# Kernel optimization log

Hardware: AMD Instinct MI355X
Metric: run time of the kernel (lower is better)

## Reference

```python
import jax, jax.numpy as jnp
import numpy as np

B, T, DM, H, DK, DV = 2, 2048, 1024, 16, 64, 64


def setup_inputs() -> dict:
    key = jax.random.key(0)
    k = jax.random.split(key, 7)
    std_k = np.float32(1.0 / np.sqrt(DK))
    std_v = np.float32(1.0 / np.sqrt(DV))
    return {
        "xq": jax.random.normal(k[0], (B, T, DM), jnp.float32),
        "xk": jax.random.normal(k[1], (B, T, DM), jnp.float32),
        "xv": jax.random.normal(k[2], (B, T, DM), jnp.float32),
        "mask": jnp.ones((B, T), jnp.float32),  # padding mask: 1 = keep
        "w_q": jax.random.normal(k[3], (H, DM, DK), jnp.float32) * std_k,
        "w_k": jax.random.normal(k[4], (H, DM, DK), jnp.float32) * std_k,
        "w_v": jax.random.normal(k[5], (H, DM, DV), jnp.float32) * std_v,
        "w_o": jax.random.normal(k[6], (H * DV, DM), jnp.float32) * np.float32(1.0 / np.sqrt(H * DV)),
        "b_o": jnp.zeros((DM,), jnp.float32),
    }


def reference(xq, xk, xv, mask, w_q, w_k, w_v, w_o, b_o):
    d_k = w_q.shape[-1]
    # per-head projections: [B,T,DM] x [H,DM,DK] -> [B,H,T,DK]
    q = jnp.einsum('bsd,hdk->bhsk', xq, w_q)
    kk = jnp.einsum('btd,hdk->bhtk', xk, w_k)
    v = jnp.einsum('btd,hdv->bhtv', xv, w_v)
    # NOTE: source divides by d_k (not sqrt(d_k)) -- kept faithful
    scores = jnp.einsum('bhsk,bhtk->bhst', q, kk) / jnp.float32(d_k)
    # _padding_mask: multiply by mask broadcast over key dim, then any exact
    # zero (masked OR coincidentally zero score) becomes -inf -- kept faithful
    masked = scores * mask[:, None, None, :]
    scores = jnp.where(masked == 0.0, -jnp.inf, masked)
    attn = jax.nn.softmax(scores, axis=-1)
    out = jnp.einsum('bhst,bhtv->bhsv', attn, v)  # [B,H,T,DV]
    b, h, t, dv = out.shape
    concat = out.transpose(0, 2, 1, 3).reshape(b, t, h * dv)
    return concat @ w_o + b_o
```

## Files before the change

### kernel.cpp

```cpp
#include <hip/hip_runtime.h>
#include <hip/hip_bf16.h>


typedef __attribute__((ext_vector_type(8))) short short8;
typedef __attribute__((ext_vector_type(4))) short short4v;
typedef __attribute__((ext_vector_type(4))) float f32x4;
typedef __attribute__((ext_vector_type(4))) int i32x4;

__device__ __forceinline__ short f2bf(float f) {
  union { float f; unsigned u; } v; v.f = f;
  unsigned r = v.u + 0x7FFFu + ((v.u >> 16) & 1u);
  return (short)(r >> 16);
}

#define GLD_LDS(g, l) __builtin_amdgcn_global_load_lds( \
    (const __attribute__((address_space(1))) void*)(g), \
    (__attribute__((address_space(3))) void*)(l), 16, 0, 0)

__global__ __launch_bounds__(256) void prep_all(
    const float* __restrict__ xq, const float* __restrict__ xk,
    const float* __restrict__ xv, const float* __restrict__ wq,
    const float* __restrict__ wk, const float* __restrict__ wv,
    const float* __restrict__ wo,
    short* __restrict__ Xb, short* __restrict__ Wall, short* __restrict__ Wot)
{
  const int bx = blockIdx.x, tid = threadIdx.x;
  __shared__ float Lt[64][65];
  if (bx < 6144) {
    int z = bx >> 11;
    const float* x = z == 0 ? xq : (z == 1 ? xk : xv);
    size_t i = ((size_t)(bx & 2047) * 256 + tid) * 8;
    f32x4 f0 = *(const f32x4*)(x + i);
    f32x4 f1 = *(const f32x4*)(x + i + 4);
    short8 s;
#pragma unroll
    for (int j = 0; j < 4; j++) { s[j] = f2bf(f0[j]); s[4 + j] = f2bf(f1[j]); }
    *(short8*)(Xb + (size_t)z * 4194304 + i) = s;
  } else if (bx < 6912) {
    int bz = bx - 6144;
    int z = bz >> 8, inner = bz & 255;
    const float* w = z == 0 ? wq : (z == 1 ? wk : wv);
    short* Wt = Wall + (size_t)z * 1048576;
    int h = inner >> 4, d0 = (inner & 15) * 64;
#pragma unroll
    for (int it = 0; it < 4; it++) {
      int e = tid + it * 256;
      int dl = e >> 4, k4 = (e & 15) * 4;
      f32x4 v = *(const f32x4*)(w + ((size_t)(h * 1024 + d0 + dl) * 64) + k4);
#pragma unroll
      for (int j = 0; j < 4; j++) Lt[dl][k4 + j] = v[j];
    }
    __syncthreads();
#pragma unroll
    for (int it = 0; it < 4; it++) {
      int e = tid + it * 256;
      int kl = e >> 4, dq = e & 15;
      short4v s;
#pragma unroll
      for (int j = 0; j < 4; j++) s[j] = f2bf(Lt[dq * 4 + j][kl]);
      *(short4v*)(Wt + (size_t)(h * 64 + kl) * 1024 + d0 + dq * 4) = s;
    }
  } else {
    int bz = bx - 6912;
    int k0 = (bz >> 4) * 64, n0 = (bz & 15) * 64;
#pragma unroll
    for (int it = 0; it < 4; it++) {
      int e = tid + it * 256;
      int kl = e >> 4, n4 = (e & 15) * 4;
      f32x4 v = *(const f32x4*)(wo + (size_t)(k0 + kl) * 1024 + n0 + n4);
#pragma unroll
      for (int j = 0; j < 4; j++) Lt[kl][n4 + j] = v[j];
    }
    __syncthreads();
#pragma unroll
    for (int it = 0; it < 4; it++) {
      int e = tid + it * 256;
      int nl = e >> 4, kq = e & 15;
      short4v s;
#pragma unroll
      for (int j = 0; j < 4; j++) s[j] = f2bf(Lt[kq * 4 + j][nl]);
      *(short4v*)(Wot + (size_t)(n0 + nl) * 1024 + k0 + kq * 4) = s;
    }
  }
}

__global__ __launch_bounds__(256) void proj_qkv3(
    const short* __restrict__ Xb, const short* __restrict__ Wall,
    short* __restrict__ Qb, short* __restrict__ Kt2, short* __restrict__ Vt2)
{
  const int z = blockIdx.z;
  const short* X  = Xb   + (size_t)z * 4194304;
  const short* Wt = Wall + (size_t)z * 1048576;

  const int t0 = blockIdx.x * 128;
  const int n0 = blockIdx.y * 128;
  const int tid = threadIdx.x, w = tid >> 6, lane = tid & 63;
  const int c = lane & 15, q4 = lane >> 4;
  const int wn = (w & 1) * 64, wt = (w >> 1) * 64;
  const int srow = lane >> 2, scol = (lane & 3) * 8;

  __shared__ __align__(16) short Al[2][2][4096];
  __shared__ __align__(16) short Bl[2][2][4096];

  f32x4 acc[4][4] = {};

#define PSTAGE(BUF, K0) do { \
    _Pragma("unroll") \
    for (int sub = 0; sub < 2; sub++) { \
      _Pragma("unroll") \
      for (int i = 0; i < 2; i++) { \
        int rg = (w * 2 + i) * 16; \
        GLD_LDS(Wt + (size_t)(n0 + rg + srow) * 1024 + (K0) + sub * 32 + scol, &Al[BUF][sub][rg * 32]); \
        GLD_LDS(X  + (size_t)(t0 + rg + srow) * 1024 + (K0) + sub * 32 + scol, &Bl[BUF][sub][rg * 32]); \
      } \
    } \
  } while (0)

#define PCOMP(BUF) do { \
    _Pragma("unroll") \
    for (int sub = 0; sub < 2; sub++) { \
      short8 a[4], bfr[4]; \
      if (z != 2) { \
        _Pragma("unroll") \
        for (int i = 0; i < 4; i++) \
          a[i] = *(const short8*)(&Al[BUF][sub][(wn + i * 16 + c) * 32 + q4 * 8]); \
        _Pragma("unroll") \
        for (int j = 0; j < 4; j++) \
          bfr[j] = *(const short8*)(&Bl[BUF][sub][(wt + j * 16 + c) * 32 + q4 * 8]); \
      } else { \
        _Pragma("unroll") \
        for (int i = 0; i < 4; i++) \
          a[i] = *(const short8*)(&Bl[BUF][sub][(wt + i * 16 + c) * 32 + q4 * 8]); \
        _Pragma("unroll") \
        for (int j = 0; j < 4; j++) \
          bfr[j] = *(const short8*)(&Al[BUF][sub][(wn + j * 16 + c) * 32 + q4 * 8]); \
      } \
      _Pragma("unroll") \
      for (int i = 0; i < 4; i++) \
        _Pragma("unroll") \
        for (int j = 0; j < 4; j++) \
          acc[i][j] = __builtin_amdgcn_mfma_f32_16x16x32_bf16(a[i], bfr[j], acc[i][j], 0, 0, 0); \
    } \
  } while (0)

  PSTAGE(0, 0);
  asm volatile("s_waitcnt vmcnt(0)" ::: "memory");
  __syncthreads();
  int cur = 0;
  for (int p = 0; p < 15; ++p) {
    PSTAGE(cur ^ 1, (p + 1) * 64);
    PCOMP(cur);
    asm volatile("s_waitcnt vmcnt(0)" ::: "memory");
    __syncthreads();
    cur ^= 1;
  }
  PCOMP(cur);
#undef PSTAGE
#undef PCOMP

  if (z != 2) {
#pragma unroll
    for (int i = 0; i < 4; i++)
#pragma unroll
      for (int j = 0; j < 4; j++) {
        int n = n0 + wn + i * 16 + q4 * 4;
        int trow = t0 + wt + j * 16 + c;
        int b = trow >> 11, t = trow & 2047;
        int h = n >> 6, cc = n & 63;
        int bh = b * 16 + h;
        f32x4 v = acc[i][j];
        short4v pk;
#pragma unroll
        for (int r = 0; r < 4; r++) pk[r] = f2bf(v[r]);
        if (z == 0) {
          *(short4v*)(Qb + (size_t)(bh * 2048 + t) * 64 + cc) = pk;
        } else {
          int t5 = t & 31, s_ = t5 >> 4, c_ = t5 & 15;
          size_t base = (size_t)bh * 131072 + (t >> 5) * 2048;
          size_t off = base + ((s_ * 2 + (cc >> 5)) * 16 + c_) * 32 +
                       ((cc >> 3) & 3) * 8 + (cc & 7);
          *(short4v*)(Kt2 + off) = pk;
        }
      }
  } else {
#pragma unroll
    for (int i = 0; i < 4; i++)
#pragma unroll
      for (int j = 0; j < 4; j++) {
        int tq = t0 + wt + i * 16 + q4 * 4;
        int n = n0 + wn + j * 16 + c;
        int b = tq >> 11, t = tq & 2047;
        int h = n >> 6, cc = n & 63;
        int bh = b * 16 + h;
        int t5 = t & 31;
        int kpb = ((t5 >> 2) & 3) * 8 + ((t5 >> 4) & 1) * 4;
        size_t base = (size_t)bh * 131072 + (t >> 5) * 2048;
        f32x4 v = acc[i][j];
        short4v pk;
#pragma unroll
        for (int r = 0; r < 4; r++) pk[r] = f2bf(v[r]);
        *(short4v*)(Vt2 + base + (size_t)cc * 32 + kpb) = pk;
      }
  }
}

__global__ __launch_bounds__(256, 2) void attn14(
    const short* __restrict__ Qb, const short* __restrict__ Kt2,
    const short* __restrict__ Vt2, const float* __restrict__ mask,
    short* __restrict__ AO)
{
  const int bh = blockIdx.x;
  const int tblk = blockIdx.y;
  const int b = bh >> 4, h = bh & 15;
  const short* Qh = Qb  + (size_t)bh * 131072;
  const short* Kh = Kt2 + (size_t)bh * 131072;
  const short* Vh = Vt2 + (size_t)bh * 131072;

  const int tid = threadIdx.x, w = tid >> 6, lane = tid & 63;
  const int c = lane & 15, q4 = lane >> 4;
  const int qrow0 = tblk * 128 + w * 32;

  __shared__ __align__(16) short KV2[2][8192];
  __shared__ __align__(16) float cmL[2048];
  __shared__ __align__(16) float cbL[2048];

  const int ch = c * 4 + q4;
  const int rdo = (ch ^ ((ch >> 3) & 3)) * 8;
  const int sch = (lane ^ ((lane >> 3) & 3)) * 8;

  {
    const float LOG2E_64c = 1.44269504088896f * 0.015625f;
    f32x4 m0 = *(const f32x4*)(mask + b * 2048 + tid * 8);
    f32x4 m1 = *(const f32x4*)(mask + b * 2048 + tid * 8 + 4);
    *(f32x4*)(&cmL[tid * 8])     = m0 * LOG2E_64c;
    *(f32x4*)(&cmL[tid * 8 + 4]) = m1 * LOG2E_64c;
    *(f32x4*)(&cbL[tid * 8])     = (m0 - 1.0f) * 240.0f;
    *(f32x4*)(&cbL[tid * 8 + 4]) = (m1 - 1.0f) * 240.0f;
  }

  short8 qa[2][2];
#pragma unroll
  for (int u = 0; u < 2; u++)
#pragma unroll
    for (int dc = 0; dc < 2; dc++)
      qa[u][dc] = *(const short8*)(Qh + (size_t)(qrow0 + u * 16 + c) * 64 + dc * 32 + q4 * 8);

  f32x4 acc[2][4] = {};
  float l[2] = {0.f, 0.f};

  const int g0 = w * 2;

#define STAGE(BI, P) do { \
    const short* s0 = (g0 < 4) ? (Kh + (size_t)(2 * (P)) * 2048 + g0 * 512) \
                               : (Vh + (size_t)(2 * (P)) * 2048 + (g0 - 4) * 512); \
    GLD_LDS(s0 + sch,         &KV2[BI][g0 * 512]); \
    GLD_LDS(s0 + 512 + sch,   &KV2[BI][g0 * 512 + 512]); \
    const short* s1 = (g0 < 4) ? (Kh + (size_t)(2 * (P) + 1) * 2048 + g0 * 512) \
                               : (Vh + (size_t)(2 * (P) + 1) * 2048 + (g0 - 4) * 512); \
    GLD_LDS(s1 + sch,         &KV2[BI][4096 + g0 * 512]); \
    GLD_LDS(s1 + 512 + sch,   &KV2[BI][4096 + g0 * 512 + 512]); \
  } while (0)

#define BODY1(KB, TT) do { \
    const short* Kb = (KB); \
    short8 kf[2][2], va[4]; \
    _Pragma("unroll") \
    for (int s = 0; s < 2; s++) \
      _Pragma("unroll") \
      for (int dc = 0; dc < 2; dc++) \
        kf[s][dc] = *(const short8*)(Kb + (s * 2 + dc) * 512 + rdo); \
    _Pragma("unroll") \
    for (int vs = 0; vs < 4; vs++) \
      va[vs] = *(const short8*)(Kb + 2048 + vs * 512 + rdo); \
    f32x4 st[2][2]; \
    _Pragma("unroll") \
    for (int u = 0; u < 2; u++) \
      _Pragma("unroll") \
      for (int s = 0; s < 2; s++) { \
        f32x4 z = {}; \
        z = __builtin_amdgcn_mfma_f32_16x16x32_bf16(kf[s][0], qa[u][0], z, 0, 0, 0); \
        st[u][s] = __builtin_amdgcn_mfma_f32_16x16x32_bf16(kf[s][1], qa[u][1], z, 0, 0, 0); \
      } \
    f32x4 cm[2], cb[2]; \
    _Pragma("unroll") \
    for (int s = 0; s < 2; s++) { \
      cm[s] = *(const f32x4*)(&cmL[(TT) * 32 + q4 * 4 + s * 16]); \
      cb[s] = *(const f32x4*)(&cbL[(TT) * 32 + q4 * 4 + s * 16]); \
    } \
    _Pragma("unroll") \
    for (int u = 0; u < 2; u++) { \
      unsigned pkd[2][2]; \
      _Pragma("unroll") \
      for (int s = 0; s < 2; s++) { \
        float e0 = __builtin_amdgcn_exp2f(st[u][s][0] * cm[s][0] + cb[s][0]); \
        float e1 = __builtin_amdgcn_exp2f(st[u][s][1] * cm[s][1] + cb[s][1]); \
        float e2 = __builtin_amdgcn_exp2f(st[u][s][2] * cm[s][2] + cb[s][2]); \
        float e3 = __builtin_amdgcn_exp2f(st[u][s][3] * cm[s][3] + cb[s][3]); \
        l[u] += (e0 + e1) + (e2 + e3); \
        unsigned p01, p23; \
        asm("v_cvt_pk_bf16_f32 %0, %1, %2" : "=v"(p01) : "v"(e0), "v"(e1)); \
        asm("v_cvt_pk_bf16_f32 %0, %1, %2" : "=v"(p23) : "v"(e2), "v"(e3)); \
        pkd[s][0] = p01; pkd[s][1] = p23; \
      } \
      union { i32x4 i; short8 s; } pb; \
      pb.i[0] = (int)pkd[0][0]; pb.i[1] = (int)pkd[0][1]; \
      pb.i[2] = (int)pkd[1][0]; pb.i[3] = (int)pkd[1][1]; \
      _Pragma("unroll") \
      for (int vs = 0; vs < 4; vs++) \
        acc[u][vs] = __builtin_amdgcn_mfma_f32_16x16x32_bf16(va[vs], pb.s, acc[u][vs], 0, 0, 0); \
    } \
  } while (0)

#define BODY(BI, P) do { \
    BODY1(&KV2[BI][0],    2 * (P)); \
    BODY1(&KV2[BI][4096], 2 * (P) + 1); \
  } while (0)

  __syncthreads();
  asm volatile("s_waitcnt vmcnt(0)" ::: "memory");
  STAGE(0, 0);
  asm volatile("s_waitcnt vmcnt(0)" ::: "memory");
  __syncthreads();
  int cur = 0;
  for (int p = 0; p < 31; ++p) {
    STAGE(cur ^ 1, p + 1);
    BODY(cur, p);
    asm volatile("s_waitcnt vmcnt(0)" ::: "memory");
    __syncthreads();
    cur ^= 1;
  }
  BODY(cur, 31);
#undef STAGE
#undef BODY1
#undef BODY

#pragma unroll
  for (int u = 0; u < 2; u++) {
    float lu = l[u];
    lu += __shfl_xor(lu, 16);
    lu += __shfl_xor(lu, 32);
    float inv = 1.0f / lu;
    size_t row = (size_t)b * 2048 + qrow0 + u * 16 + c;
#pragma unroll
    for (int vs = 0; vs < 4; vs++) {
      f32x4 v = acc[u][vs];
      short4v pk;
#pragma unroll
      for (int r = 0; r < 4; r++) pk[r] = f2bf(v[r] * inv);
      *(short4v*)(AO + row * 1024 + h * 64 + vs * 16 + q4 * 4) = pk;
    }
  }
}

__global__ __launch_bounds__(256) void out_proj3(
    const short* __restrict__ AO, const short* __restrict__ Wot,
    const float* __restrict__ bo, float* __restrict__ out)
{
  const int t0 = blockIdx.x * 128;
  const int n0 = blockIdx.y * 128;
  const int tid = threadIdx.x, w = tid >> 6, lane = tid & 63;
  const int c = lane & 15, q4 = lane >> 4;
  const int wn = (w & 1) * 64, wt = (w >> 1) * 64;
  const int srow = lane >> 2, scol = (lane & 3) * 8;

  __shared__ __align__(16) short Al[2][2][4096];
  __shared__ __align__(16) short Bl[2][2][4096];

  f32x4 acc[4][4] = {};

#define PSTAGE(BUF, K0) do { \
    _Pragma("unroll") \
    for (int sub = 0; sub < 2; sub++) { \
      _Pragma("unroll") \
      for (int i = 0; i < 2; i++) { \
        int rg = (w * 2 + i) * 16; \
        GLD_LDS(Wot + (size_t)(n0 + rg + srow) * 1024 + (K0) + sub * 32 + scol, &Al[BUF][sub][rg * 32]); \
        GLD_LDS(AO  + (size_t)(t0 + rg + srow) * 1024 + (K0) + sub * 32 + scol, &Bl[BUF][sub][rg * 32]); \
      } \
    } \
  } while (0)

#define PCOMP(BUF) do { \
    _Pragma("unroll") \
    for (int sub = 0; sub < 2; sub++) { \
      short8 a[4], bfr[4]; \
      _Pragma("unroll") \
      for (int i = 0; i < 4; i++) \
        a[i] = *(const short8*)(&Al[BUF][sub][(wn + i * 16 + c) * 32 + q4 * 8]); \
      _Pragma("unroll") \
      for (int j = 0; j < 4; j++) \
        bfr[j] = *(const short8*)(&Bl[BUF][sub][(wt + j * 16 + c) * 32 + q4 * 8]); \
      _Pragma("unroll") \
      for (int i = 0; i < 4; i++) \
        _Pragma("unroll") \
        for (int j = 0; j < 4; j++) \
          acc[i][j] = __builtin_amdgcn_mfma_f32_16x16x32_bf16(a[i], bfr[j], acc[i][j], 0, 0, 0); \
    } \
  } while (0)

  PSTAGE(0, 0);
  asm volatile("s_waitcnt vmcnt(0)" ::: "memory");
  __syncthreads();
  int cur = 0;
  for (int p = 0; p < 15; ++p) {
    PSTAGE(cur ^ 1, (p + 1) * 64);
    PCOMP(cur);
    asm volatile("s_waitcnt vmcnt(0)" ::: "memory");
    __syncthreads();
    cur ^= 1;
  }
  PCOMP(cur);
#undef PSTAGE
#undef PCOMP

#pragma unroll
  for (int i = 0; i < 4; i++)
#pragma unroll
    for (int j = 0; j < 4; j++) {
      int n = n0 + wn + i * 16 + q4 * 4;
      int trow = t0 + wt + j * 16 + c;
      f32x4 v = acc[i][j] + *(const f32x4*)(bo + n);
      *(f32x4*)(out + (size_t)trow * 1024 + n) = v;
    }
}

extern "C" void kernel_launch(void* const* d_in, const int* in_sizes, int n_in,
                              void* d_out, int out_size, void* d_ws, size_t ws_size,
                              hipStream_t stream)
{
  (void)in_sizes; (void)n_in; (void)out_size; (void)ws_size;
  const float* xq   = (const float*)d_in[0];
  const float* xk   = (const float*)d_in[1];
  const float* xv   = (const float*)d_in[2];
  const float* mask = (const float*)d_in[3];
  const float* wq   = (const float*)d_in[4];
  const float* wk   = (const float*)d_in[5];
  const float* wv   = (const float*)d_in[6];
  const float* wo   = (const float*)d_in[7];
  const float* bo   = (const float*)d_in[8];
  float* out = (float*)d_out;

  char* ws = (char*)d_ws;
  short* Wall = (short*)(ws + (size_t)0);
  short* Wot  = (short*)(ws + ((size_t)6 << 20));
  short* Xb   = (short*)(ws + ((size_t)8 << 20));
  short* AO   = (short*)(ws + ((size_t)8 << 20));
  short* Qb   = (short*)(ws + ((size_t)32 << 20));
  short* Kt2  = (short*)(ws + ((size_t)40 << 20));
  short* Vt2  = (short*)(ws + ((size_t)48 << 20));

  prep_all<<<7168, 256, 0, stream>>>(xq, xk, xv, wq, wk, wv, wo, Xb, Wall, Wot);
  proj_qkv3<<<dim3(32, 8, 3), 256, 0, stream>>>(Xb, Wall, Qb, Kt2, Vt2);
  attn14<<<dim3(32, 16), 256, 0, stream>>>(Qb, Kt2, Vt2, mask, AO);
  out_proj3<<<dim3(32, 8), 256, 0, stream>>>(AO, Wot, bo, out);
}
```

Before: 217.9 us.

## Fuse fp32-to-bf16 activation conversion into QKV projection staging

Removes the separate activation conversion pass from the prep kernel and instead loads fp32 activations directly in the projection GEMM. They go into registers, are converted with packed bf16 instructions, and are written to LDS after the MFMA compute, which keeps the double-buffered pipeline. This avoids writing and re-reading a 24MB bf16 copy of the inputs. In exchange each projection block reads fp32 activations (twice the bytes) once per N-tile, across 8 N-tiles. It also uses more registers and no longer uses async global-to-LDS loads for the X operand.

```diff
diff --git a/kernel.cpp b/kernel.cpp
--- a/kernel.cpp
+++ b/kernel.cpp
@@ -17,28 +17,15 @@
     (const __attribute__((address_space(1))) void*)(g), \
     (__attribute__((address_space(3))) void*)(l), 16, 0, 0)
 
-__global__ __launch_bounds__(256) void prep_all(
-    const float* __restrict__ xq, const float* __restrict__ xk,
-    const float* __restrict__ xv, const float* __restrict__ wq,
-    const float* __restrict__ wk, const float* __restrict__ wv,
-    const float* __restrict__ wo,
-    short* __restrict__ Xb, short* __restrict__ Wall, short* __restrict__ Wot)
+__global__ __launch_bounds__(256) void prep_w(
+    const float* __restrict__ wq, const float* __restrict__ wk,
+    const float* __restrict__ wv, const float* __restrict__ wo,
+    short* __restrict__ Wall, short* __restrict__ Wot)
 {
   const int bx = blockIdx.x, tid = threadIdx.x;
   __shared__ float Lt[64][65];
-  if (bx < 6144) {
-    int z = bx >> 11;
-    const float* x = z == 0 ? xq : (z == 1 ? xk : xv);
-    size_t i = ((size_t)(bx & 2047) * 256 + tid) * 8;
-    f32x4 f0 = *(const f32x4*)(x + i);
-    f32x4 f1 = *(const f32x4*)(x + i + 4);
-    short8 s;
-#pragma unroll
-    for (int j = 0; j < 4; j++) { s[j] = f2bf(f0[j]); s[4 + j] = f2bf(f1[j]); }
-    *(short8*)(Xb + (size_t)z * 4194304 + i) = s;
-  } else if (bx < 6912) {
-    int bz = bx - 6144;
-    int z = bz >> 8, inner = bz & 255;
+  if (bx < 768) {
+    int z = bx >> 8, inner = bx & 255;
     const float* w = z == 0 ? wq : (z == 1 ? wk : wv);
     short* Wt = Wall + (size_t)z * 1048576;
     int h = inner >> 4, d0 = (inner & 15) * 64;
@@ -61,7 +48,7 @@
       *(short4v*)(Wt + (size_t)(h * 64 + kl) * 1024 + d0 + dq * 4) = s;
     }
   } else {
-    int bz = bx - 6912;
+    int bz = bx - 768;
     int k0 = (bz >> 4) * 64, n0 = (bz & 15) * 64;
 #pragma unroll
     for (int it = 0; it < 4; it++) {
@@ -84,12 +71,13 @@
   }
 }
 
-__global__ __launch_bounds__(256) void proj_qkv3(
-    const short* __restrict__ Xb, const short* __restrict__ Wall,
+__global__ __launch_bounds__(256) void proj_qkv4(
+    const float* __restrict__ xq, const float* __restrict__ xk,
+    const float* __restrict__ xv, const short* __restrict__ Wall,
     short* __restrict__ Qb, short* __restrict__ Kt2, short* __restrict__ Vt2)
 {
   const int z = blockIdx.z;
-  const short* X  = Xb   + (size_t)z * 4194304;
+  const float* X  = z == 0 ? xq : (z == 1 ? xk : xv);
   const short* Wt = Wall + (size_t)z * 1048576;
 
   const int t0 = blockIdx.x * 128;
@@ -103,15 +91,44 @@
   __shared__ __align__(16) short Bl[2][2][4096];
 
   f32x4 acc[4][4] = {};
-
-#define PSTAGE(BUF, K0) do { \
+  f32x4 xr[2][2][2];
+
+#define PSTAGE_A(BUF, K0) do { \
     _Pragma("unroll") \
     for (int sub = 0; sub < 2; sub++) { \
       _Pragma("unroll") \
       for (int i = 0; i < 2; i++) { \
         int rg = (w * 2 + i) * 16; \
         GLD_LDS(Wt + (size_t)(n0 + rg + srow) * 1024 + (K0) + sub * 32 + scol, &Al[BUF][sub][rg * 32]); \
-        GLD_LDS(X  + (size_t)(t0 + rg + srow) * 1024 + (K0) + sub * 32 + scol, &Bl[BUF][sub][rg * 32]); \
+      } \
+    } \
+  } while (0)
+
+#define XLOAD(K0) do { \
+    _Pragma("unroll") \
+    for (int i = 0; i < 2; i++) { \
+      _Pragma("unroll") \
+      for (int sub = 0; sub < 2; sub++) { \
+        const float* xs = X + (size_t)(t0 + (w * 2 + i) * 16 + srow) * 1024 + (K0) + sub * 32 + scol; \
+        xr[i][sub][0] = *(const f32x4*)(xs); \
+        xr[i][sub][1] = *(const f32x4*)(xs + 4); \
+      } \
+    } \
+  } while (0)
+
+#define XWRITE(BUF) do { \
+    _Pragma("unroll") \
+    for (int i = 0; i < 2; i++) { \
+      _Pragma("unroll") \
+      for (int sub = 0; sub < 2; sub++) { \
+        unsigned p0, p1, p2, p3; \
+        asm("v_cvt_pk_bf16_f32 %0, %1, %2" : "=v"(p0) : "v"(xr[i][sub][0][0]), "v"(xr[i][sub][0][1])); \
+        asm("v_cvt_pk_bf16_f32 %0, %1, %2" : "=v"(p1) : "v"(xr[i][sub][0][2]), "v"(xr[i][sub][0][3])); \
+        asm("v_cvt_pk_bf16_f32 %0, %1, %2" : "=v"(p2) : "v"(xr[i][sub][1][0]), "v"(xr[i][sub][1][1])); \
+        asm("v_cvt_pk_bf16_f32 %0, %1, %2" : "=v"(p3) : "v"(xr[i][sub][1][2]), "v"(xr[i][sub][1][3])); \
+        union { i32x4 iv; short8 s; } pk; \
+        pk.iv[0] = (int)p0; pk.iv[1] = (int)p1; pk.iv[2] = (int)p2; pk.iv[3] = (int)p3; \
+        *(short8*)(&Bl[BUF][sub][((w * 2 + i) * 16 + srow) * 32 + scol]) = pk.s; \
       } \
     } \
   } while (0)
@@ -143,19 +160,25 @@
     } \
   } while (0)
 
-  PSTAGE(0, 0);
+  PSTAGE_A(0, 0);
+  XLOAD(0);
+  XWRITE(0);
   asm volatile("s_waitcnt vmcnt(0)" ::: "memory");
   __syncthreads();
   int cur = 0;
   for (int p = 0; p < 15; ++p) {
-    PSTAGE(cur ^ 1, (p + 1) * 64);
+    PSTAGE_A(cur ^ 1, (p + 1) * 64);
+    XLOAD((p + 1) * 64);
     PCOMP(cur);
+    XWRITE(cur ^ 1);
     asm volatile("s_waitcnt vmcnt(0)" ::: "memory");
     __syncthreads();
     cur ^= 1;
   }
   PCOMP(cur);
-#undef PSTAGE
+#undef PSTAGE_A
+#undef XLOAD
+#undef XWRITE
 #undef PCOMP
 
   if (z != 2) {
@@ -443,14 +466,13 @@
   char* ws = (char*)d_ws;
   short* Wall = (short*)(ws + (size_t)0);
   short* Wot  = (short*)(ws + ((size_t)6 << 20));
-  short* Xb   = (short*)(ws + ((size_t)8 << 20));
   short* AO   = (short*)(ws + ((size_t)8 << 20));
-  short* Qb   = (short*)(ws + ((size_t)32 << 20));
-  short* Kt2  = (short*)(ws + ((size_t)40 << 20));
-  short* Vt2  = (short*)(ws + ((size_t)48 << 20));
-
-  prep_all<<<7168, 256, 0, stream>>>(xq, xk, xv, wq, wk, wv, wo, Xb, Wall, Wot);
-  proj_qkv3<<<dim3(32, 8, 3), 256, 0, stream>>>(Xb, Wall, Qb, Kt2, Vt2);
+  short* Qb   = (short*)(ws + ((size_t)16 << 20));
+  short* Kt2  = (short*)(ws + ((size_t)24 << 20));
+  short* Vt2  = (short*)(ws + ((size_t)32 << 20));
+
+  prep_w<<<1024, 256, 0, stream>>>(wq, wk, wv, wo, Wall, Wot);
+  proj_qkv4<<<dim3(32, 8, 3), 256, 0, stream>>>(xq, xk, xv, Wall, Qb, Kt2, Vt2);
   attn14<<<dim3(32, 16), 256, 0, stream>>>(Qb, Kt2, Vt2, mask, AO);
   out_proj3<<<dim3(32, 8), 256, 0, stream>>>(AO, Wot, bo, out);
 }
```

Result: slower. 239.8 us (+10.0%).
